# Optimization experiments

Measured on AMD Instinct MI355X. Metric: run time of the kernel, lower is better.

## Reference

```python
import jax, jax.numpy as jnp
import numpy as np

B, N, D = 4, 4096, 256


def setup_inputs() -> dict:
    key = jax.random.key(0)
    k1, k2 = jax.random.split(key)
    val = jax.random.normal(k1, (B, N, D), dtype=jnp.float32)
    state = jax.random.normal(k2, (B, N), dtype=jnp.float32)
    return {"val": val, "state": state}


def reference(val, state):
    # pairwise_fn: scaled dot-product -> scores [B, N, N]
    scale = val.shape[-1] ** -0.5
    scores = jnp.einsum("bid,bjd->bij", val, val) * scale
    # edge_compress_fn = softsign (non-softmax compression)
    edges = scores / (1.0 + jnp.abs(scores))
    # state_weight_edges=False, val/state projections are Identity
    delta_state = jnp.einsum("bij,bj->bi", edges, state)   # [B, N]
    delta_val = jnp.einsum("bij,bjd->bid", edges, val)      # [B, N, D]
    return (delta_state, delta_val)
```

## Files before the change

### kernel.cpp

```cpp
#include <hip/hip_runtime.h>


#define B_  4
#define N_  4096
#define D_  256

typedef __attribute__((ext_vector_type(8))) short short8;
typedef __attribute__((ext_vector_type(4))) float floatx4;

__device__ __forceinline__ unsigned short f2bf(float f) {
    unsigned int u = __float_as_uint(f);
    u += 0x7fff + ((u >> 16) & 1);
    return (unsigned short)(u >> 16);
}

__device__ __forceinline__ void gl_lds16(const void* g, void* l) {
    __builtin_amdgcn_global_load_lds(
        (const __attribute__((address_space(1))) unsigned int*)g,
        (__attribute__((address_space(3))) unsigned int*)l, 16, 0, 0);
}
__device__ __forceinline__ void gl_lds4(const void* g, void* l) {
    __builtin_amdgcn_global_load_lds(
        (const __attribute__((address_space(1))) unsigned int*)g,
        (__attribute__((address_space(3))) unsigned int*)l, 4, 0, 0);
}

__global__ __launch_bounds__(256)
void prepass_kernel(const float* __restrict__ val,
                    unsigned short* __restrict__ Vb,
                    unsigned short* __restrict__ VT) {
    __shared__ unsigned short tile[64][68];
    const int t   = threadIdx.x;
    const int blk = blockIdx.x;
    const int b   = blk >> 8;
    const int it  = (blk >> 2) & 63;
    const int dt  = blk & 3;
    const int i0  = it * 64, d0 = dt * 64;
    const float*    vb  = val + (size_t)b * N_ * D_;
    unsigned short* Vbb = Vb  + (size_t)b * N_ * D_;
    unsigned short* VTb = VT  + (size_t)b * D_ * N_;

    #pragma unroll
    for (int q = 0; q < 4; ++q) {
        int idx = t + 256 * q;
        int row = idx >> 4;
        int c4  = idx & 15;
        float4 v = *(const float4*)(vb + (size_t)(i0 + row) * D_ + d0 + c4 * 4);
        ushort4 h;
        h.x = f2bf(v.x); h.y = f2bf(v.y); h.z = f2bf(v.z); h.w = f2bf(v.w);
        *(ushort4*)(Vbb + (size_t)(i0 + row) * D_ + d0 + c4 * 4) = h;
        *(ushort4*)&tile[row][c4 * 4] = h;
    }
    __syncthreads();
    #pragma unroll
    for (int q = 0; q < 4; ++q) {
        int dr = (t >> 4) + q * 16;
        int i4 = t & 15;
        ushort4 h;
        h.x = tile[i4 * 4 + 0][dr];
        h.y = tile[i4 * 4 + 1][dr];
        h.z = tile[i4 * 4 + 2][dr];
        h.w = tile[i4 * 4 + 3][dr];
        *(ushort4*)(VTb + (size_t)(d0 + dr) * N_ + i0 + i4 * 4) = h;
    }
}

__global__ __launch_bounds__(256, 2)
void prop_main(const float* __restrict__ state,
               const unsigned short* __restrict__ Vb,
               const unsigned short* __restrict__ VT,
               float* __restrict__ dvout,
               float* __restrict__ dsout,
               int split) {
    __shared__ __attribute__((aligned(16))) unsigned short vj[64 * 256];
    __shared__ __attribute__((aligned(16))) unsigned short vjt[16384];
    __shared__ __attribute__((aligned(16))) unsigned short Esh[64][72];
    __shared__ float stj[64];
    __shared__ float dsred[2][64];

    const int t    = threadIdx.x;
    const int w    = t >> 6;
    const int lane = t & 63;
    const int quad = lane >> 4;
    const int l16  = lane & 15;

    int b, it0, h, niter;
    if (split) {
        h   = blockIdx.x & 1;
        it0 = ((blockIdx.x >> 1) & 63) << 6;
        b   = blockIdx.x >> 7;
        niter = 32;
    } else {
        h   = 0;
        it0 = (blockIdx.x & 63) << 6;
        b   = blockIdx.x >> 6;
        niter = 64;
    }
    const int jbase = h * 2048;

    const unsigned short* Vbb = Vb + (size_t)b * N_ * D_;
    const unsigned short* VTb = VT + (size_t)b * D_ * N_;
    const float*          stb = state + (size_t)b * N_;

    const int hi  = lane >> 5;
    const int p32 = lane & 31;
    const int dr8 = lane >> 3;
    const int p8  = lane & 7;

    int vgoff[8];
    int tgoff[8];
    #pragma unroll
    for (int n = 0; n < 8; ++n) {
        int r = 2 * (w * 8 + n) + hi;
        int g = p32 ^ (r & 7);
        vgoff[n] = r * 256 + g * 8;
        int d = 8 * (w * 8 + n) + dr8;
        int gt = p8 ^ dr8;
        tgoff[n] = d * 4096 + gt * 8;
    }

    const int r0 = (w >> 1) * 32;
    const int c0 = (w & 1) * 32;
    const int pA = l16 & 7;

    short8 A0[8], A1[8];
    {
        const unsigned short* ar0 = Vbb + (size_t)(it0 + r0 + l16) * 256 + quad * 8;
        const unsigned short* ar1 = ar0 + 16 * 256;
        #pragma unroll
        for (int ks = 0; ks < 8; ++ks) {
            A0[ks] = *(const short8*)(ar0 + ks * 32);
            A1[ks] = *(const short8*)(ar1 + ks * 32);
        }
    }

    #pragma unroll
    for (int n = 0; n < 8; ++n)
        gl_lds16(Vbb + (size_t)jbase * 256 + vgoff[n], &vj[(w * 8 + n) * 512]);
    if (w == 0) gl_lds4(stb + jbase + lane, &stj[0]);
    #pragma unroll
    for (int n = 0; n < 8; ++n)
        gl_lds16(VTb + (size_t)jbase + tgoff[n], &vjt[(w * 8 + n) * 512]);

    floatx4 dv[4][4];
    #pragma unroll
    for (int a = 0; a < 4; ++a)
        #pragma unroll
        for (int c = 0; c < 4; ++c)
            dv[a][c] = (floatx4){0.f, 0.f, 0.f, 0.f};
    float dsp[8];
    #pragma unroll
    for (int k = 0; k < 8; ++k) dsp[k] = 0.f;

    for (int k = 0; k < niter; ++k) {
        __syncthreads();

        floatx4 sa[2][2];
        #pragma unroll
        for (int a = 0; a < 2; ++a)
            #pragma unroll
            for (int c = 0; c < 2; ++c)
                sa[a][c] = (floatx4){0.f, 0.f, 0.f, 0.f};

        #pragma unroll
        for (int ks = 0; ks < 8; ++ks) {
            const int p = ((ks * 4 + quad) ^ pA) * 8;
            short8 b0 = *(const short8*)&vj[(c0 + l16) * 256 + p];
            short8 b1 = *(const short8*)&vj[(c0 + 16 + l16) * 256 + p];
            sa[0][0] = __builtin_amdgcn_mfma_f32_16x16x32_bf16(A0[ks], b0, sa[0][0], 0, 0, 0);
            sa[0][1] = __builtin_amdgcn_mfma_f32_16x16x32_bf16(A0[ks], b1, sa[0][1], 0, 0, 0);
            sa[1][0] = __builtin_amdgcn_mfma_f32_16x16x32_bf16(A1[ks], b0, sa[1][0], 0, 0, 0);
            sa[1][1] = __builtin_amdgcn_mfma_f32_16x16x32_bf16(A1[ks], b1, sa[1][1], 0, 0, 0);
        }

        float stc0 = stj[c0 + l16];
        float stc1 = stj[c0 + 16 + l16];
        #pragma unroll
        for (int a = 0; a < 2; ++a) {
            #pragma unroll
            for (int r = 0; r < 4; ++r) {
                const int il = r0 + a * 16 + quad * 4 + r;
                float s0 = sa[a][0][r] * 0.0625f;
                float s1 = sa[a][1][r] * 0.0625f;
                float e0 = s0 * __builtin_amdgcn_rcpf(1.0f + fabsf(s0));
                float e1 = s1 * __builtin_amdgcn_rcpf(1.0f + fabsf(s1));
                dsp[a * 4 + r] += e0 * stc0 + e1 * stc1;
                Esh[il][c0 + l16]      = f2bf(e0);
                Esh[il][c0 + 16 + l16] = f2bf(e1);
            }
        }
        __syncthreads();

        if (k + 1 < niter) {
            const size_t j0n = jbase + (size_t)(k + 1) * 64;
            #pragma unroll
            for (int n = 0; n < 8; ++n)
                gl_lds16(Vbb + j0n * 256 + vgoff[n], &vj[(w * 8 + n) * 512]);
            if (w == 0) gl_lds4(stb + j0n + lane, &stj[0]);
        }

        #pragma unroll
        for (int ks = 0; ks < 2; ++ks) {
            short8 af[4], bfr[4];
            #pragma unroll
            for (int a2 = 0; a2 < 4; ++a2)
                af[a2] = *(const short8*)&Esh[a2 * 16 + l16][ks * 32 + quad * 8];
            #pragma unroll
            for (int c2 = 0; c2 < 4; ++c2) {
                const int d = w * 64 + c2 * 16 + l16;
                const int p = ((ks * 4 + quad) ^ (l16 & 7)) * 8;
                bfr[c2] = *(const short8*)&vjt[d * 64 + p];
            }
            #pragma unroll
            for (int a2 = 0; a2 < 4; ++a2)
                #pragma unroll
                for (int c2 = 0; c2 < 4; ++c2)
                    dv[a2][c2] = __builtin_amdgcn_mfma_f32_16x16x32_bf16(af[a2], bfr[c2], dv[a2][c2], 0, 0, 0);
        }
        __syncthreads();

        if (k + 1 < niter) {
            const size_t j0n = jbase + (size_t)(k + 1) * 64;
            #pragma unroll
            for (int n = 0; n < 8; ++n)
                gl_lds16(VTb + j0n + tgoff[n], &vjt[(w * 8 + n) * 512]);
        }
    }

    float* dvo = dvout + (size_t)h * B_ * N_ * D_ + (size_t)b * N_ * D_;
    #pragma unroll
    for (int a2 = 0; a2 < 4; ++a2)
        #pragma unroll
        for (int c2 = 0; c2 < 4; ++c2)
            #pragma unroll
            for (int r = 0; r < 4; ++r) {
                const int i = it0 + a2 * 16 + quad * 4 + r;
                const int d = w * 64 + c2 * 16 + l16;
                dvo[(size_t)i * D_ + d] = dv[a2][c2][r];
            }

    #pragma unroll
    for (int k = 0; k < 8; ++k) {
        float v = dsp[k];
        v += __shfl_xor(v, 1);
        v += __shfl_xor(v, 2);
        v += __shfl_xor(v, 4);
        v += __shfl_xor(v, 8);
        dsp[k] = v;
    }
    if (l16 == 0) {
        #pragma unroll
        for (int a = 0; a < 2; ++a)
            #pragma unroll
            for (int r = 0; r < 4; ++r) {
                const int row = (w >> 1) * 32 + a * 16 + quad * 4 + r;
                dsred[w & 1][row] = dsp[a * 4 + r];
            }
    }
    __syncthreads();
    if (t < 64)
        dsout[(size_t)h * B_ * N_ + (size_t)b * N_ + it0 + t] = dsred[0][t] + dsred[1][t];
}

__global__ __launch_bounds__(256)
void combine_kernel(const float4* __restrict__ dv0, const float4* __restrict__ dv1,
                    const float*  __restrict__ ds0, const float*  __restrict__ ds1,
                    float* __restrict__ out) {
    const int NDV4 = B_ * N_ * D_ / 4;
    const int NDS  = B_ * N_;
    int x = blockIdx.x * 256 + threadIdx.x;
    if (x < NDV4) {
        float4 a = dv0[x], c = dv1[x];
        float4 r;
        r.x = a.x + c.x; r.y = a.y + c.y; r.z = a.z + c.z; r.w = a.w + c.w;
        ((float4*)(out + NDS))[x] = r;
    } else {
        int y = (x - NDV4) * 4;
        if (y < NDS) {
            float4 a = *(const float4*)(ds0 + y);
            float4 c = *(const float4*)(ds1 + y);
            float4 r;
            r.x = a.x + c.x; r.y = a.y + c.y; r.z = a.z + c.z; r.w = a.w + c.w;
            *(float4*)(out + y) = r;
        }
    }
}

__global__ __launch_bounds__(256, 1)
void prop_kernel_fb(const float* __restrict__ val,
                    const float* __restrict__ state,
                    float* __restrict__ out) {
    __shared__ __attribute__((aligned(16))) unsigned short vi[64][264];
    __shared__ __attribute__((aligned(16))) unsigned short vj[64][264];
    __shared__ __attribute__((aligned(16))) unsigned short vjt[2048][8];
    __shared__ __attribute__((aligned(16))) unsigned short Esh[64][72];
    __shared__ float stj[64];
    __shared__ float dsred[2][64];

    const int t    = threadIdx.x;
    const int w    = t >> 6;
    const int lane = t & 63;
    const int quad = lane >> 4;
    const int l16  = lane & 15;
    const int b   = blockIdx.x >> 6;
    const int it0 = (blockIdx.x & 63) << 6;
    const float* valb = val   + (size_t)b * N_ * D_;
    const float* stb  = state + (size_t)b * N_;

    #pragma unroll
    for (int n = 0; n < 16; ++n) {
        int idx = t + 256 * n;
        int row = idx >> 6;
        int c4  = idx & 63;
        float4 v = *(const float4*)(valb + (size_t)(it0 + row) * D_ + c4 * 4);
        ushort4 h;
        h.x = f2bf(v.x); h.y = f2bf(v.y); h.z = f2bf(v.z); h.w = f2bf(v.w);
        *(ushort4*)&vi[row][c4 * 4] = h;
    }

    const int r0 = (w >> 1) * 32;
    const int c0 = (w & 1) * 32;
    floatx4 dv[4][4];
    #pragma unroll
    for (int a = 0; a < 4; ++a)
        #pragma unroll
        for (int c = 0; c < 4; ++c)
            dv[a][c] = (floatx4){0.f, 0.f, 0.f, 0.f};
    float dsp[8];
    #pragma unroll
    for (int k = 0; k < 8; ++k) dsp[k] = 0.f;

    for (int jt = 0; jt < 64; ++jt) {
        const int j0 = jt * 64;
        #pragma unroll
        for (int n = 0; n < 16; ++n) {
            int idx = t + 256 * n;
            int row = idx >> 6;
            int c4  = idx & 63;
            float4 v = *(const float4*)(valb + (size_t)(j0 + row) * D_ + c4 * 4);
            ushort4 h;
            h.x = f2bf(v.x); h.y = f2bf(v.y); h.z = f2bf(v.z); h.w = f2bf(v.w);
            *(ushort4*)&vj[row][c4 * 4] = h;
        }
        if (t < 64) stj[t] = stb[j0 + t];
        __syncthreads();

        #pragma unroll
        for (int n = 0; n < 8; ++n) {
            const int d  = t;
            const int jb = n;
            short8 pk;
            #pragma unroll
            for (int jj = 0; jj < 8; ++jj) pk[jj] = (short)vj[jb * 8 + jj][d];
            *(short8*)&vjt[d * 8 + (jb ^ (d & 7))][0] = pk;
        }

        floatx4 sa[2][2];
        #pragma unroll
        for (int a = 0; a < 2; ++a)
            #pragma unroll
            for (int c = 0; c < 2; ++c)
                sa[a][c] = (floatx4){0.f, 0.f, 0.f, 0.f};
        #pragma unroll
        for (int ks = 0; ks < 8; ++ks) {
            const int d0 = ks * 32 + quad * 8;
            short8 a0 = *(const short8*)&vi[r0 + l16][d0];
            short8 a1 = *(const short8*)&vi[r0 + 16 + l16][d0];
            short8 b0 = *(const short8*)&vj[c0 + l16][d0];
            short8 b1 = *(const short8*)&vj[c0 + 16 + l16][d0];
            sa[0][0] = __builtin_amdgcn_mfma_f32_16x16x32_bf16(a0, b0, sa[0][0], 0, 0, 0);
            sa[0][1] = __builtin_amdgcn_mfma_f32_16x16x32_bf16(a0, b1, sa[0][1], 0, 0, 0);
            sa[1][0] = __builtin_amdgcn_mfma_f32_16x16x32_bf16(a1, b0, sa[1][0], 0, 0, 0);
            sa[1][1] = __builtin_amdgcn_mfma_f32_16x16x32_bf16(a1, b1, sa[1][1], 0, 0, 0);
        }

        float stc0 = stj[c0 + l16];
        float stc1 = stj[c0 + 16 + l16];
        #pragma unroll
        for (int a = 0; a < 2; ++a) {
            #pragma unroll
            for (int r = 0; r < 4; ++r) {
                const int il = r0 + a * 16 + quad * 4 + r;
                float s0 = sa[a][0][r] * 0.0625f;
                float s1 = sa[a][1][r] * 0.0625f;
                float e0 = s0 / (1.0f + fabsf(s0));
                float e1 = s1 / (1.0f + fabsf(s1));
                dsp[a * 4 + r] += e0 * stc0 + e1 * stc1;
                Esh[il][c0 + l16]      = f2bf(e0);
                Esh[il][c0 + 16 + l16] = f2bf(e1);
            }
        }
        __syncthreads();

        #pragma unroll
        for (int ks = 0; ks < 2; ++ks) {
            short8 af[4], bfr[4];
            #pragma unroll
            for (int a2 = 0; a2 < 4; ++a2)
                af[a2] = *(const short8*)&Esh[a2 * 16 + l16][ks * 32 + quad * 8];
            #pragma unroll
            for (int c2 = 0; c2 < 4; ++c2) {
                const int d  = w * 64 + c2 * 16 + l16;
                const int jb = ks * 4 + quad;
                bfr[c2] = *(const short8*)&vjt[d * 8 + (jb ^ (d & 7))][0];
            }
            #pragma unroll
            for (int a2 = 0; a2 < 4; ++a2)
                #pragma unroll
                for (int c2 = 0; c2 < 4; ++c2)
                    dv[a2][c2] = __builtin_amdgcn_mfma_f32_16x16x32_bf16(af[a2], bfr[c2], dv[a2][c2], 0, 0, 0);
        }
    }

    float* dvo = out + (size_t)B_ * N_ + (size_t)b * N_ * D_;
    #pragma unroll
    for (int a2 = 0; a2 < 4; ++a2)
        #pragma unroll
        for (int c2 = 0; c2 < 4; ++c2)
            #pragma unroll
            for (int r = 0; r < 4; ++r) {
                const int i = it0 + a2 * 16 + quad * 4 + r;
                const int d = w * 64 + c2 * 16 + l16;
                dvo[(size_t)i * D_ + d] = dv[a2][c2][r];
            }

    #pragma unroll
    for (int k = 0; k < 8; ++k) {
        float v = dsp[k];
        v += __shfl_xor(v, 1);
        v += __shfl_xor(v, 2);
        v += __shfl_xor(v, 4);
        v += __shfl_xor(v, 8);
        dsp[k] = v;
    }
    if (l16 == 0) {
        #pragma unroll
        for (int a = 0; a < 2; ++a)
            #pragma unroll
            for (int r = 0; r < 4; ++r) {
                const int row = (w >> 1) * 32 + a * 16 + quad * 4 + r;
                dsred[w & 1][row] = dsp[a * 4 + r];
            }
    }
    __syncthreads();
    if (t < 64) out[(size_t)b * N_ + it0 + t] = dsred[0][t] + dsred[1][t];
}

extern "C" void kernel_launch(void* const* d_in, const int* in_sizes, int n_in,
                              void* d_out, int out_size, void* d_ws, size_t ws_size,
                              hipStream_t stream) {
    const float* val   = (const float*)d_in[0];
    const float* state = (const float*)d_in[1];
    float* out = (float*)d_out;

    const size_t nE        = (size_t)B_ * N_ * D_;
    const size_t need_base = 2 * nE * sizeof(unsigned short);
    const size_t need_split = need_base + 2 * nE * sizeof(float)
                            + 2 * (size_t)B_ * N_ * sizeof(float);

    if (ws_size >= need_base) {
        unsigned short* Vb = (unsigned short*)d_ws;
        unsigned short* VT = Vb + nE;
        prepass_kernel<<<dim3(1024), dim3(256), 0, stream>>>(val, Vb, VT);
        if (ws_size >= need_split) {
            float* dvp = (float*)(VT + nE);
            float* dsp = dvp + 2 * nE;
            prop_main<<<dim3(512), dim3(256), 0, stream>>>(state, Vb, VT, dvp, dsp, 1);
            const int NDV4 = B_ * N_ * D_ / 4;
            const int NDS4 = B_ * N_ / 4;
            combine_kernel<<<dim3((NDV4 + NDS4) / 256), dim3(256), 0, stream>>>(
                (const float4*)dvp, (const float4*)(dvp + nE),
                dsp, dsp + (size_t)B_ * N_, out);
        } else {
            prop_main<<<dim3(256), dim3(256), 0, stream>>>(
                state, Vb, VT, out + (size_t)B_ * N_, out, 0);
        }
    } else {
        prop_kernel_fb<<<dim3(256), dim3(256), 0, stream>>>(val, state, out);
    }
}
```

Before: 162.7 us.

## Share j-tiles across two row groups in 512-thread blocks with double-buffered VT

```diff
diff --git a/kernel.cpp b/kernel.cpp
--- a/kernel.cpp
+++ b/kernel.cpp
@@ -65,38 +65,35 @@
     }
 }
 
-__global__ __launch_bounds__(256, 2)
+__global__ __launch_bounds__(512, 1)
 void prop_main(const float* __restrict__ state,
                const unsigned short* __restrict__ Vb,
                const unsigned short* __restrict__ VT,
-               float* __restrict__ dvout,
-               float* __restrict__ dsout,
-               int split) {
-    __shared__ __attribute__((aligned(16))) unsigned short vj[64 * 256];
-    __shared__ __attribute__((aligned(16))) unsigned short vjt[16384];
-    __shared__ __attribute__((aligned(16))) unsigned short Esh[64][72];
-    __shared__ float stj[64];
-    __shared__ float dsred[2][64];
+               float* __restrict__ dvp,
+               float* __restrict__ dsp_o)
+{
+    __shared__ __attribute__((aligned(16))) unsigned char smem[136448];
 
     const int t    = threadIdx.x;
+    const int g    = t >> 8;
     const int w    = t >> 6;
+    const int w4   = w & 3;
     const int lane = t & 63;
     const int quad = lane >> 4;
     const int l16  = lane & 15;
 
-    int b, it0, h, niter;
-    if (split) {
-        h   = blockIdx.x & 1;
-        it0 = ((blockIdx.x >> 1) & 63) << 6;
-        b   = blockIdx.x >> 7;
-        niter = 32;
-    } else {
-        h   = 0;
-        it0 = (blockIdx.x & 63) << 6;
-        b   = blockIdx.x >> 6;
-        niter = 64;
-    }
-    const int jbase = h * 2048;
+    const int x   = blockIdx.x;
+    const int b   = x >> 6;
+    const int it  = (x >> 1) & 31;
+    const int jh  = x & 1;
+    const int it0 = it * 128;
+    const int jbase = jh * 2048;
+    const int niter = 32;
+
+    unsigned short* vjL  = (unsigned short*)(smem + 65536);
+    unsigned short* stjL_= (unsigned short*)(smem + 135168);
+    float*          stjL = (float*)stjL_;
+    float*          dsredg = (float*)(smem + 135424 + g * 512);
 
     const unsigned short* Vbb = Vb + (size_t)b * N_ * D_;
     const unsigned short* VTb = VT + (size_t)b * D_ * N_;
@@ -107,25 +104,25 @@
     const int dr8 = lane >> 3;
     const int p8  = lane & 7;
 
-    int vgoff[8];
-    int tgoff[8];
-    #pragma unroll
-    for (int n = 0; n < 8; ++n) {
-        int r = 2 * (w * 8 + n) + hi;
-        int g = p32 ^ (r & 7);
-        vgoff[n] = r * 256 + g * 8;
-        int d = 8 * (w * 8 + n) + dr8;
+    int vgoff[4];
+    int tgoff[4];
+    #pragma unroll
+    for (int n = 0; n < 4; ++n) {
+        int r  = 2 * (w * 4 + n) + hi;
+        int gr = p32 ^ (r & 7);
+        vgoff[n] = r * 256 + gr * 8;
+        int d  = 8 * (w * 4 + n) + dr8;
         int gt = p8 ^ dr8;
         tgoff[n] = d * 4096 + gt * 8;
     }
 
-    const int r0 = (w >> 1) * 32;
-    const int c0 = (w & 1) * 32;
+    const int r0 = (w4 >> 1) * 32;
+    const int c0 = (w4 & 1) * 32;
     const int pA = l16 & 7;
 
     short8 A0[8], A1[8];
     {
-        const unsigned short* ar0 = Vbb + (size_t)(it0 + r0 + l16) * 256 + quad * 8;
+        const unsigned short* ar0 = Vbb + (size_t)(it0 + g * 64 + r0 + l16) * 256 + quad * 8;
         const unsigned short* ar1 = ar0 + 16 * 256;
         #pragma unroll
         for (int ks = 0; ks < 8; ++ks) {
@@ -135,12 +132,14 @@
     }
 
     #pragma unroll
-    for (int n = 0; n < 8; ++n)
-        gl_lds16(Vbb + (size_t)jbase * 256 + vgoff[n], &vj[(w * 8 + n) * 512]);
-    if (w == 0) gl_lds4(stb + jbase + lane, &stj[0]);
-    #pragma unroll
-    for (int n = 0; n < 8; ++n)
-        gl_lds16(VTb + (size_t)jbase + tgoff[n], &vjt[(w * 8 + n) * 512]);
+    for (int n = 0; n < 4; ++n)
+        gl_lds16(VTb + (size_t)jbase + tgoff[n],
+                 smem + (w * 4 + n) * 1024);
+    #pragma unroll
+    for (int n = 0; n < 4; ++n)
+        gl_lds16(Vbb + (size_t)jbase * 256 + vgoff[n],
+                 smem + 65536 + (w * 4 + n) * 1024);
+    if (w == 0) gl_lds4(stb + jbase + lane, stjL);
 
     floatx4 dv[4][4];
     #pragma unroll
@@ -153,7 +152,19 @@
     for (int k = 0; k < 8; ++k) dsp[k] = 0.f;
 
     for (int k = 0; k < niter; ++k) {
+        const int buf = k & 1;
+        unsigned short* Eshg = (unsigned short*)(smem + 98304 + g * 18432 + buf * 9216);
+        unsigned short* vjtg = (unsigned short*)(smem + buf * 32768);
+
         __syncthreads();
+
+        if (k + 1 < niter) {
+            const size_t j0n = jbase + (size_t)(k + 1) * 64;
+            #pragma unroll
+            for (int n = 0; n < 4; ++n)
+                gl_lds16(VTb + j0n + tgoff[n],
+                         smem + (buf ^ 1) * 32768 + (w * 4 + n) * 1024);
+        }
 
         floatx4 sa[2][2];
         #pragma unroll
@@ -165,28 +176,28 @@
         #pragma unroll
         for (int ks = 0; ks < 8; ++ks) {
             const int p = ((ks * 4 + quad) ^ pA) * 8;
-            short8 b0 = *(const short8*)&vj[(c0 + l16) * 256 + p];
-            short8 b1 = *(const short8*)&vj[(c0 + 16 + l16) * 256 + p];
+            short8 b0 = *(const short8*)&vjL[(c0 + l16) * 256 + p];
+            short8 b1 = *(const short8*)&vjL[(c0 + 16 + l16) * 256 + p];
             sa[0][0] = __builtin_amdgcn_mfma_f32_16x16x32_bf16(A0[ks], b0, sa[0][0], 0, 0, 0);
             sa[0][1] = __builtin_amdgcn_mfma_f32_16x16x32_bf16(A0[ks], b1, sa[0][1], 0, 0, 0);
             sa[1][0] = __builtin_amdgcn_mfma_f32_16x16x32_bf16(A1[ks], b0, sa[1][0], 0, 0, 0);
             sa[1][1] = __builtin_amdgcn_mfma_f32_16x16x32_bf16(A1[ks], b1, sa[1][1], 0, 0, 0);
         }
 
-        float stc0 = stj[c0 + l16];
-        float stc1 = stj[c0 + 16 + l16];
+        float stc0 = stjL[c0 + l16];
+        float stc1 = stjL[c0 + 16 + l16];
         #pragma unroll
         for (int a = 0; a < 2; ++a) {
             #pragma unroll
             for (int r = 0; r < 4; ++r) {
                 const int il = r0 + a * 16 + quad * 4 + r;
-                float s0 = sa[a][0][r] * 0.0625f;
-                float s1 = sa[a][1][r] * 0.0625f;
-                float e0 = s0 * __builtin_amdgcn_rcpf(1.0f + fabsf(s0));
-                float e1 = s1 * __builtin_amdgcn_rcpf(1.0f + fabsf(s1));
+                float s0 = sa[a][0][r];
+                float s1 = sa[a][1][r];
+                float e0 = s0 * __builtin_amdgcn_rcpf(16.0f + fabsf(s0));
+                float e1 = s1 * __builtin_amdgcn_rcpf(16.0f + fabsf(s1));
                 dsp[a * 4 + r] += e0 * stc0 + e1 * stc1;
-                Esh[il][c0 + l16]      = f2bf(e0);
-                Esh[il][c0 + 16 + l16] = f2bf(e1);
+                Eshg[il * 72 + c0 + l16]      = f2bf(e0);
+                Eshg[il * 72 + c0 + 16 + l16] = f2bf(e1);
             }
         }
         __syncthreads();
@@ -194,9 +205,10 @@
         if (k + 1 < niter) {
             const size_t j0n = jbase + (size_t)(k + 1) * 64;
             #pragma unroll
-            for (int n = 0; n < 8; ++n)
-                gl_lds16(Vbb + j0n * 256 + vgoff[n], &vj[(w * 8 + n) * 512]);
-            if (w == 0) gl_lds4(stb + j0n + lane, &stj[0]);
+            for (int n = 0; n < 4; ++n)
+                gl_lds16(Vbb + j0n * 256 + vgoff[n],
+                         smem + 65536 + (w * 4 + n) * 1024);
+            if (w == 0) gl_lds4(stb + j0n + lane, stjL);
         }
 
         #pragma unroll
@@ -204,12 +216,12 @@
             short8 af[4], bfr[4];
             #pragma unroll
             for (int a2 = 0; a2 < 4; ++a2)
-                af[a2] = *(const short8*)&Esh[a2 * 16 + l16][ks * 32 + quad * 8];
+                af[a2] = *(const short8*)&Eshg[(a2 * 16 + l16) * 72 + ks * 32 + quad * 8];
             #pragma unroll
             for (int c2 = 0; c2 < 4; ++c2) {
-                const int d = w * 64 + c2 * 16 + l16;
+                const int d = w4 * 64 + c2 * 16 + l16;
                 const int p = ((ks * 4 + quad) ^ (l16 & 7)) * 8;
-                bfr[c2] = *(const short8*)&vjt[d * 64 + p];
+                bfr[c2] = *(const short8*)&vjtg[d * 64 + p];
             }
             #pragma unroll
             for (int a2 = 0; a2 < 4; ++a2)
@@ -217,26 +229,19 @@
                 for (int c2 = 0; c2 < 4; ++c2)
                     dv[a2][c2] = __builtin_amdgcn_mfma_f32_16x16x32_bf16(af[a2], bfr[c2], dv[a2][c2], 0, 0, 0);
         }
-        __syncthreads();
-
-        if (k + 1 < niter) {
-            const size_t j0n = jbase + (size_t)(k + 1) * 64;
-            #pragma unroll
-            for (int n = 0; n < 8; ++n)
-                gl_lds16(VTb + j0n + tgoff[n], &vjt[(w * 8 + n) * 512]);
-        }
-    }
-
-    float* dvo = dvout + (size_t)h * B_ * N_ * D_ + (size_t)b * N_ * D_;
+    }
+
+    float* dvo = dvp + (size_t)jh * B_ * N_ * D_ + (size_t)b * N_ * D_
+                     + (size_t)(it0 + g * 64) * D_;
     #pragma unroll
     for (int a2 = 0; a2 < 4; ++a2)
         #pragma unroll
         for (int c2 = 0; c2 < 4; ++c2)
             #pragma unroll
             for (int r = 0; r < 4; ++r) {
-                const int i = it0 + a2 * 16 + quad * 4 + r;
-                const int d = w * 64 + c2 * 16 + l16;
-                dvo[(size_t)i * D_ + d] = dv[a2][c2][r];
+                const int il = a2 * 16 + quad * 4 + r;
+                const int d  = w4 * 64 + c2 * 16 + l16;
+                dvo[(size_t)il * D_ + d] = dv[a2][c2][r];
             }
 
     #pragma unroll
@@ -253,13 +258,18 @@
         for (int a = 0; a < 2; ++a)
             #pragma unroll
             for (int r = 0; r < 4; ++r) {
-                const int row = (w >> 1) * 32 + a * 16 + quad * 4 + r;
-                dsred[w & 1][row] = dsp[a * 4 + r];
+                const int row = r0 + a * 16 + quad * 4 + r;
+                dsredg[(w4 & 1) * 64 + row] = dsp[a * 4 + r];
             }
     }
     __syncthreads();
-    if (t < 64)
-        dsout[(size_t)h * B_ * N_ + (size_t)b * N_ + it0 + t] = dsred[0][t] + dsred[1][t];
+    if (t < 128) {
+        const int gg  = t >> 6;
+        const int row = t & 63;
+        const float* dsr = (const float*)(smem + 135424 + gg * 512);
+        dsp_o[(size_t)jh * B_ * N_ + (size_t)b * N_ + it0 + gg * 64 + row]
+            = dsr[row] + dsr[64 + row];
+    }
 }
 
 __global__ __launch_bounds__(256)
@@ -453,28 +463,23 @@
     const float* state = (const float*)d_in[1];
     float* out = (float*)d_out;
 
-    const size_t nE        = (size_t)B_ * N_ * D_;
-    const size_t need_base = 2 * nE * sizeof(unsigned short);
+    const size_t nE         = (size_t)B_ * N_ * D_;
+    const size_t need_base  = 2 * nE * sizeof(unsigned short);
     const size_t need_split = need_base + 2 * nE * sizeof(float)
                             + 2 * (size_t)B_ * N_ * sizeof(float);
 
-    if (ws_size >= need_base) {
+    if (ws_size >= need_split) {
         unsigned short* Vb = (unsigned short*)d_ws;
         unsigned short* VT = Vb + nE;
+        float* dvp = (float*)(VT + nE);
+        float* dsp = dvp + 2 * nE;
         prepass_kernel<<<dim3(1024), dim3(256), 0, stream>>>(val, Vb, VT);
-        if (ws_size >= need_split) {
-            float* dvp = (float*)(VT + nE);
-            float* dsp = dvp + 2 * nE;
-            prop_main<<<dim3(512), dim3(256), 0, stream>>>(state, Vb, VT, dvp, dsp, 1);
-            const int NDV4 = B_ * N_ * D_ / 4;
-            const int NDS4 = B_ * N_ / 4;
-            combine_kernel<<<dim3((NDV4 + NDS4) / 256), dim3(256), 0, stream>>>(
-                (const float4*)dvp, (const float4*)(dvp + nE),
-                dsp, dsp + (size_t)B_ * N_, out);
-        } else {
-            prop_main<<<dim3(256), dim3(256), 0, stream>>>(
-                state, Vb, VT, out + (size_t)B_ * N_, out, 0);
-        }
+        prop_main<<<dim3(256), dim3(512), 0, stream>>>(state, Vb, VT, dvp, dsp);
+        const int NDV4 = B_ * N_ * D_ / 4;
+        const int NDS4 = B_ * N_ / 4;
+        combine_kernel<<<dim3((NDV4 + NDS4) / 256), dim3(256), 0, stream>>>(
+            (const float4*)dvp, (const float4*)(dvp + nE),
+            dsp, dsp + (size_t)B_ * N_, out);
     } else {
         prop_kernel_fb<<<dim3(256), dim3(256), 0, stream>>>(val, state, out);
     }
```

New measurement: 151.0 us. -7.2%, faster.
